# Kernel optimization log

Hardware: AMD Instinct MI355X
Metric: run time of the kernel (lower is better)

Reference implementation:

```python
import jax, jax.numpy as jnp
import numpy as np

D_MODEL, EMB_DIM, ORDER, SEQ_LEN, BATCH = 768, 33, 64, 8192, 2


def setup_inputs() -> dict:
    key = jax.random.key(0)
    ks = jax.random.split(key, 9)
    x = jax.random.normal(ks[0], (BATCH, D_MODEL, SEQ_LEN), dtype=jnp.float32)

    # PositionalEmbedding: t in [0,1], complex exponential bands
    bands = (EMB_DIM - 1) // 2
    t = jnp.linspace(0.0, 1.0, SEQ_LEN, dtype=jnp.float32)[None, :, None]          # (1, L, 1)
    t_rescaled = jnp.linspace(0.0, SEQ_LEN - 1, SEQ_LEN, dtype=jnp.float32)[None, :, None]
    w_ang = 2.0 * jnp.pi * t_rescaled / SEQ_LEN                                     # (1, L, 1)
    f = jnp.linspace(1e-4, bands - 1, bands, dtype=jnp.float32)[None, None]         # (1, 1, bands)
    zc = jnp.exp(-1j * f.astype(jnp.complex64) * w_ang.astype(jnp.complex64))
    z = jnp.concatenate([t, zc.real, zc.imag], axis=-1)                             # (1, L, emb_dim)

    # Sin activation frequency (shared single instance across all MLP layers), w=1
    freq = jnp.ones((1, ORDER), dtype=jnp.float32)

    def lin(k, fan_out, fan_in):
        s = 1.0 / np.sqrt(fan_in)
        return jax.random.normal(k, (fan_out, fan_in), dtype=jnp.float32) * s

    W1 = lin(ks[1], ORDER, EMB_DIM)
    b1 = jax.random.normal(ks[2], (ORDER,), dtype=jnp.float32) * 0.02
    W2 = lin(ks[3], ORDER, ORDER)
    b2 = jax.random.normal(ks[4], (ORDER,), dtype=jnp.float32) * 0.02
    W3 = lin(ks[5], ORDER, ORDER)
    b3 = jax.random.normal(ks[6], (ORDER,), dtype=jnp.float32) * 0.02
    Wout = lin(ks[7], D_MODEL, ORDER)  # no bias

    # ExponentialModulation deltas (deterministic buffer)
    target, fast_pct, slow_pct = 0.01, 0.3, 1.5
    max_decay = np.log(target) / fast_pct
    min_decay = np.log(target) / slow_pct
    deltas = jnp.linspace(min_decay, max_decay, D_MODEL, dtype=jnp.float32)[None, None]  # (1,1,d)

    bias_D = jax.random.normal(ks[8], (D_MODEL,), dtype=jnp.float32)

    return {"x": x, "L": SEQ_LEN, "z": z, "t": t, "freq": freq,
            "W1": W1, "b1": b1, "W2": W2, "b2": b2, "W3": W3, "b3": b3,
            "Wout": Wout, "deltas": deltas, "bias_D": bias_D}


def reference(x, L, z, t, freq, W1, b1, W2, b2, W3, b3, Wout, deltas, bias_D):
    zL, tL = z[:, :L], t[:, :L]                      # (1, L, emb_dim), (1, L, 1)
    # Implicit filter MLP with shared Sin activation
    h = jnp.sin(freq * (jnp.einsum('ble,oe->blo', zL, W1) + b1))
    h = jnp.sin(freq * (jnp.einsum('blo,po->blp', h, W2) + b2))
    h = jnp.sin(freq * (jnp.einsum('blo,po->blp', h, W3) + b3))
    h = jnp.einsum('blo,do->bld', h, Wout)           # (1, L, d_model)
    # Exponential modulation
    h = h * jnp.exp(-tL * jnp.abs(deltas))
    k = h[0].T                                       # (d_model, L)
    # FFT-based long convolution (fftconv_ref with gelu=False).
    # torch: k_f = rfft(k, n)/n ; y = irfft(u_f*k_f, n, norm='forward') == standard irfft(u_f*rfft(k,n), n)
    fft_size = 2 * L
    k_f = jnp.fft.rfft(k, n=fft_size)                # (d_model, n//2+1) complex
    u_f = jnp.fft.rfft(x, n=fft_size)                # (B, d_model, n//2+1)
    y = jnp.fft.irfft(u_f * k_f, n=fft_size)[..., :L]
    out = y + x * bias_D[:, None]
    return out.astype(x.dtype)
```

## Files before the change

### kernel.cpp

```cpp
#include <hip/hip_runtime.h>
#include <hip/hip_fp16.h>
#include <math.h>

#define D_MODEL 768
#define EMB 33
#define ORDER 64
#define SEQ 8192
#define BATCH 2
#define M 8192

#define PI_F 3.14159265358979323846f

#define IDX(a) ((a) + ((a) >> 4) + ((a) >> 7))
#define LDS_SZ 8768

__device__ __forceinline__ int rev13(int x) { return (int)(__brev((unsigned)x) >> 19); }

__device__ __constant__ float C8[8] = {
    1.f, 0.9238795325f, 0.7071067812f, 0.3826834324f,
    0.f, -0.3826834324f, -0.7071067812f, -0.9238795325f };
__device__ __constant__ float S8n[8] = {
    0.f, -0.3826834324f, -0.7071067812f, -0.9238795325f,
    -1.f, -0.9238795325f, -0.7071067812f, -0.3826834324f };
__device__ __constant__ float S8p[8] = {
    0.f, 0.3826834324f, 0.7071067812f, 0.9238795325f,
    1.f, 0.9238795325f, 0.7071067812f, 0.3826834324f };

__global__ __launch_bounds__(256) void mlp_kernel(
    const float* __restrict__ z, const float* __restrict__ freq,
    const float* __restrict__ W1, const float* __restrict__ b1,
    const float* __restrict__ W2, const float* __restrict__ b2,
    const float* __restrict__ W3, const float* __restrict__ b3,
    float* __restrict__ h3T)
{
    __shared__ float zt[33 * 72];
    __shared__ float h1[64 * 72];
    __shared__ float h2[64 * 72];
    __shared__ float Wb[64 * 68];
    __shared__ float sfr[64], sb[64];
    int t = threadIdx.x;
    int l0 = blockIdx.x * 64;

    for (int i = t; i < 64 * 33; i += 256) {
        int l = i / 33, e = i - l * 33;
        zt[e * 72 + l] = z[(size_t)(l0 + l) * 33 + e];
    }
    for (int i = t; i < 64 * 33; i += 256) {
        int o = i / 33, e = i - o * 33;
        Wb[e * 68 + o] = W1[i];
    }
    if (t < 64) { sfr[t] = freq[t]; sb[t] = b1[t]; }
    __syncthreads();

    int lx = t & 15, oy = t >> 4;
    float fr4[4], bi4[4], acc[4][4];
#pragma unroll
    for (int i = 0; i < 4; ++i) { fr4[i] = sfr[4 * oy + i]; bi4[i] = sb[4 * oy + i]; }
#pragma unroll
    for (int c = 0; c < 4; ++c)
#pragma unroll
        for (int i = 0; i < 4; ++i) acc[c][i] = bi4[i];
    for (int e = 0; e < 33; ++e) {
        float4 hv = *(const float4*)&zt[e * 72 + 4 * lx];
        float4 wv = *(const float4*)&Wb[e * 68 + 4 * oy];
        float h[4] = {hv.x, hv.y, hv.z, hv.w}, w[4] = {wv.x, wv.y, wv.z, wv.w};
#pragma unroll
        for (int c = 0; c < 4; ++c)
#pragma unroll
            for (int i = 0; i < 4; ++i) acc[c][i] = fmaf(h[c], w[i], acc[c][i]);
    }
#pragma unroll
    for (int i = 0; i < 4; ++i) {
        float4 v = make_float4(__sinf(fr4[i] * acc[0][i]), __sinf(fr4[i] * acc[1][i]),
                               __sinf(fr4[i] * acc[2][i]), __sinf(fr4[i] * acc[3][i]));
        *(float4*)&h1[(4 * oy + i) * 72 + 4 * lx] = v;
    }
    __syncthreads();

    for (int i = t; i < 4096; i += 256) {
        int o = i >> 6, q = i & 63;
        Wb[q * 68 + o] = W2[i];
    }
    if (t < 64) sb[t] = b2[t];
    __syncthreads();
#pragma unroll
    for (int i = 0; i < 4; ++i) bi4[i] = sb[4 * oy + i];
#pragma unroll
    for (int c = 0; c < 4; ++c)
#pragma unroll
        for (int i = 0; i < 4; ++i) acc[c][i] = bi4[i];
    for (int q = 0; q < 64; ++q) {
        float4 hv = *(const float4*)&h1[q * 72 + 4 * lx];
        float4 wv = *(const float4*)&Wb[q * 68 + 4 * oy];
        float h[4] = {hv.x, hv.y, hv.z, hv.w}, w[4] = {wv.x, wv.y, wv.z, wv.w};
#pragma unroll
        for (int c = 0; c < 4; ++c)
#pragma unroll
            for (int i = 0; i < 4; ++i) acc[c][i] = fmaf(h[c], w[i], acc[c][i]);
    }
#pragma unroll
    for (int i = 0; i < 4; ++i) {
        float4 v = make_float4(__sinf(fr4[i] * acc[0][i]), __sinf(fr4[i] * acc[1][i]),
                               __sinf(fr4[i] * acc[2][i]), __sinf(fr4[i] * acc[3][i]));
        *(float4*)&h2[(4 * oy + i) * 72 + 4 * lx] = v;
    }
    __syncthreads();

    for (int i = t; i < 4096; i += 256) {
        int o = i >> 6, q = i & 63;
        Wb[q * 68 + o] = W3[i];
    }
    if (t < 64) sb[t] = b3[t];
    __syncthreads();
#pragma unroll
    for (int i = 0; i < 4; ++i) bi4[i] = sb[4 * oy + i];
#pragma unroll
    for (int c = 0; c < 4; ++c)
#pragma unroll
        for (int i = 0; i < 4; ++i) acc[c][i] = bi4[i];
    for (int q = 0; q < 64; ++q) {
        float4 hv = *(const float4*)&h2[q * 72 + 4 * lx];
        float4 wv = *(const float4*)&Wb[q * 68 + 4 * oy];
        float h[4] = {hv.x, hv.y, hv.z, hv.w}, w[4] = {wv.x, wv.y, wv.z, wv.w};
#pragma unroll
        for (int c = 0; c < 4; ++c)
#pragma unroll
            for (int i = 0; i < 4; ++i) acc[c][i] = fmaf(h[c], w[i], acc[c][i]);
    }
#pragma unroll
    for (int i = 0; i < 4; ++i) {
        float4 v = make_float4(__sinf(fr4[i] * acc[0][i]), __sinf(fr4[i] * acc[1][i]),
                               __sinf(fr4[i] * acc[2][i]), __sinf(fr4[i] * acc[3][i]));
        *(float4*)&h3T[(size_t)(4 * oy + i) * SEQ + l0 + 4 * lx] = v;
    }
}

__global__ __launch_bounds__(256) void filt_kernel(
    const float* __restrict__ h3T, const float* __restrict__ Wout,
    const float* __restrict__ tvec, const float* __restrict__ deltas,
    float* __restrict__ kout)
{
    __shared__ float ht[64 * 132];
    __shared__ float wt[64 * 68];
    int t = threadIdx.x;
    int l0 = blockIdx.x * 128, d0 = blockIdx.y * 64;

    for (int i = t; i < 64 * 128; i += 256) {
        int o = i >> 7, l = i & 127;
        ht[o * 132 + l] = h3T[(size_t)o * SEQ + l0 + l];
    }
    for (int i = t; i < 4096; i += 256) {
        int dd = i >> 6, kk = i & 63;
        wt[kk * 68 + dd] = Wout[(size_t)(d0 + dd) * 64 + kk];
    }
    __syncthreads();

    int lx = t & 31, dy = t >> 5;
    float acc[4][8];
#pragma unroll
    for (int c = 0; c < 4; ++c)
#pragma unroll
        for (int i = 0; i < 8; ++i) acc[c][i] = 0.f;
    for (int kk = 0; kk < 64; ++kk) {
        float4 hv = *(const float4*)&ht[kk * 132 + 4 * lx];
        float4 w0 = *(const float4*)&wt[kk * 68 + 8 * dy];
        float4 w1 = *(const float4*)&wt[kk * 68 + 8 * dy + 4];
        float h[4] = {hv.x, hv.y, hv.z, hv.w};
        float w[8] = {w0.x, w0.y, w0.z, w0.w, w1.x, w1.y, w1.z, w1.w};
#pragma unroll
        for (int c = 0; c < 4; ++c)
#pragma unroll
            for (int i = 0; i < 8; ++i) acc[c][i] = fmaf(h[c], w[i], acc[c][i]);
    }

    float4 tl4 = *(const float4*)&tvec[l0 + 4 * lx];
    float tl[4] = {tl4.x, tl4.y, tl4.z, tl4.w};
    float del[8];
#pragma unroll
    for (int i = 0; i < 8; ++i) del[i] = fabsf(deltas[d0 + 8 * dy + i]);
#pragma unroll
    for (int i = 0; i < 8; ++i) {
        int d = d0 + 8 * dy + i;
        float4 v = make_float4(acc[0][i] * __expf(-tl[0] * del[i]),
                               acc[1][i] * __expf(-tl[1] * del[i]),
                               acc[2][i] * __expf(-tl[2] * del[i]),
                               acc[3][i] * __expf(-tl[3] * del[i]));
        *(float4*)&kout[(size_t)d * SEQ + l0 + 4 * lx] = v;
    }
}

template<int H>
__device__ __forceinline__ void fwd8(float2* A, int t)
{
    constexpr int H4 = H / 4;
    int j0 = t & (H4 - 1);
    float c1, s1;
    __sincosf((-PI_F / (float)H) * (float)j0, &s1, &c1);
#pragma unroll
    for (int gg = 0; gg < 2; ++gg) {
        int g = t + (gg << 9);
        int j = g & (H4 - 1);
        int i = ((g & ~(H4 - 1)) << 3) | j;
        float c1g = c1, s1g = s1;
        if (H4 > 512 && gg == 1) {
            const float cR = 0.9238795325f, sR = -0.3826834324f;
            c1g = c1 * cR - s1 * sR;
            s1g = s1 * cR + c1 * sR;
        }
        float c2 = c1g * c1g - s1g * s1g, s2 = 2.f * c1g * s1g;
        float c3 = c2 * c2 - s2 * s2,     s3 = 2.f * c2 * s2;
        float xr[8], xi[8];
        int ad[8];
#pragma unroll
        for (int m = 0; m < 8; ++m) {
            ad[m] = IDX(i + m * H4);
            float2 v = A[ad[m]];
            xr[m] = v.x; xi[m] = v.y;
        }
        const float r = 0.70710678118f;
        float twc[4], tws[4];
        twc[0] = c1g;             tws[0] = s1g;
        twc[1] = r * (c1g + s1g); tws[1] = r * (s1g - c1g);
        twc[2] = s1g;             tws[2] = -c1g;
        twc[3] = r * (s1g - c1g); tws[3] = -r * (c1g + s1g);
#pragma unroll
        for (int m = 0; m < 4; ++m) {
            float ur = xr[m] + xr[m + 4], ui = xi[m] + xi[m + 4];
            float dr = xr[m] - xr[m + 4], di = xi[m] - xi[m + 4];
            xr[m] = ur; xi[m] = ui;
            xr[m + 4] = dr * twc[m] - di * tws[m];
            xi[m + 4] = dr * tws[m] + di * twc[m];
        }
#pragma unroll
        for (int base = 0; base < 8; base += 4)
#pragma unroll
            for (int mm = 0; mm < 2; ++mm) {
                int a = base + mm, b = a + 2;
                float ur = xr[a] + xr[b], ui = xi[a] + xi[b];
                float dr = xr[a] - xr[b], di = xi[a] - xi[b];
                xr[a] = ur; xi[a] = ui;
                if (mm == 0) { xr[b] = dr * c2 - di * s2; xi[b] = dr * s2 + di * c2; }
                else         { xr[b] = dr * s2 + di * c2; xi[b] = di * s2 - dr * c2; }
            }
#pragma unroll
        for (int m = 0; m < 8; m += 2) {
            float ur = xr[m] + xr[m + 1], ui = xi[m] + xi[m + 1];
            float dr = xr[m] - xr[m + 1], di = xi[m] - xi[m + 1];
            xr[m] = ur; xi[m] = ui;
            xr[m + 1] = dr * c3 - di * s3; xi[m + 1] = dr * s3 + di * c3;
        }
#pragma unroll
        for (int m = 0; m < 8; ++m) A[ad[m]] = make_float2(xr[m], xi[m]);
    }
}

template<int H>
__device__ __forceinline__ void inv8(float2* A, int t)
{
    int j0 = t & (H - 1);
    float ct, st;
    __sincosf((PI_F / (float)(4 * H)) * (float)j0, &st, &ct);
#pragma unroll
    for (int gg = 0; gg < 2; ++gg) {
        int g = t + (gg << 9);
        int j = g & (H - 1);
        int i = ((g & ~(H - 1)) << 3) | j;
        float c = ct, s = st;
        if (H > 512 && gg == 1) {
            const float cR = 0.9238795325f, sR = 0.3826834324f;
            c = ct * cR - st * sR;
            s = st * cR + ct * sR;
        }
        float c2 = c * c - s * s, s2 = 2.f * c * s;
        float c4 = c2 * c2 - s2 * s2, s4 = 2.f * c2 * s2;
        float xr[8], xi[8]; int ad[8];
#pragma unroll
        for (int m = 0; m < 8; ++m) {
            ad[m] = IDX(i + m * H);
            float2 v = A[ad[m]];
            xr[m] = v.x; xi[m] = v.y;
        }
#pragma unroll
        for (int m = 0; m < 8; m += 2) {
            float tr = xr[m + 1] * c4 - xi[m + 1] * s4;
            float ti = xr[m + 1] * s4 + xi[m + 1] * c4;
            xr[m + 1] = xr[m] - tr; xi[m + 1] = xi[m] - ti;
            xr[m]     = xr[m] + tr; xi[m]     = xi[m] + ti;
        }
#pragma unroll
        for (int base = 0; base < 8; base += 4)
#pragma unroll
            for (int mm = 0; mm < 2; ++mm) {
                int a = base + mm, b = a + 2;
                float tr, ti;
                if (mm == 0) { tr = xr[b] * c2 - xi[b] * s2; ti = xr[b] * s2 + xi[b] * c2; }
                else         { tr = -(xr[b] * s2 + xi[b] * c2); ti = xr[b] * c2 - xi[b] * s2; }
                xr[b] = xr[a] - tr; xi[b] = xi[a] - ti;
                xr[a] = xr[a] + tr; xi[a] = xi[a] + ti;
            }
        const float r = 0.70710678118f;
        float t3c[4], t3s[4];
        t3c[0] = c;           t3s[0] = s;
        t3c[1] = r * (c - s); t3s[1] = r * (c + s);
        t3c[2] = -s;          t3s[2] = c;
        t3c[3] = -r * (c + s); t3s[3] = r * (c - s);
#pragma unroll
        for (int m = 0; m < 4; ++m) {
            float tr = xr[m + 4] * t3c[m] - xi[m + 4] * t3s[m];
            float ti = xr[m + 4] * t3s[m] + xi[m + 4] * t3c[m];
            xr[m + 4] = xr[m] - tr; xi[m + 4] = xi[m] - ti;
            xr[m]     = xr[m] + tr; xi[m]     = xi[m] + ti;
        }
#pragma unroll
        for (int m = 0; m < 8; ++m) A[ad[m]] = make_float2(xr[m], xi[m]);
    }
}

__device__ __forceinline__ void fft_fwd(float2* A, int t)
{
    fwd8<4096>(A, t); __syncthreads();
    fwd8<512>(A, t);  __syncthreads();
    fwd8<64>(A, t);   __syncthreads();
    {
        int pb = IDX(16 * t);
        float fr[16], fi[16];
#pragma unroll
        for (int e = 0; e < 16; ++e) { float2 v = A[pb + e]; fr[e] = v.x; fi[e] = v.y; }
#pragma unroll
        for (int k = 0; k < 8; ++k) {
            float cs = C8[k], sn = S8n[k];
            float arr = fr[k], aii = fi[k], brr = fr[k + 8], bii = fi[k + 8];
            fr[k] = arr + brr; fi[k] = aii + bii;
            float dr = arr - brr, di = aii - bii;
            fr[k + 8] = dr * cs - di * sn; fi[k + 8] = dr * sn + di * cs;
        }
#pragma unroll
        for (int b0 = 0; b0 < 16; b0 += 8)
#pragma unroll
            for (int k = 0; k < 4; ++k) {
                float cs = C8[2 * k], sn = S8n[2 * k];
                int i0 = b0 + k, i1 = i0 + 4;
                float arr = fr[i0], aii = fi[i0], brr = fr[i1], bii = fi[i1];
                fr[i0] = arr + brr; fi[i0] = aii + bii;
                float dr = arr - brr, di = aii - bii;
                fr[i1] = dr * cs - di * sn; fi[i1] = dr * sn + di * cs;
            }
#pragma unroll
        for (int b0 = 0; b0 < 16; b0 += 4)
#pragma unroll
            for (int k = 0; k < 2; ++k) {
                float cs = C8[4 * k], sn = S8n[4 * k];
                int i0 = b0 + k, i1 = i0 + 2;
                float arr = fr[i0], aii = fi[i0], brr = fr[i1], bii = fi[i1];
                fr[i0] = arr + brr; fi[i0] = aii + bii;
                float dr = arr - brr, di = aii - bii;
                fr[i1] = dr * cs - di * sn; fi[i1] = dr * sn + di * cs;
            }
#pragma unroll
        for (int b0 = 0; b0 < 16; b0 += 2) {
            float arr = fr[b0], aii = fi[b0], brr = fr[b0 + 1], bii = fi[b0 + 1];
            fr[b0] = arr + brr; fi[b0] = aii + bii;
            fr[b0 + 1] = arr - brr; fi[b0 + 1] = aii - bii;
        }
#pragma unroll
        for (int e = 0; e < 16; ++e) A[pb + e] = make_float2(fr[e], fi[e]);
        __syncthreads();
    }
}

__device__ __forceinline__ void fft_inv(float2* A, int t)
{
    {
        int pb = IDX(16 * t);
        float fr[16], fi[16];
#pragma unroll
        for (int e = 0; e < 16; ++e) { float2 v = A[pb + e]; fr[e] = v.x; fi[e] = v.y; }
#pragma unroll
        for (int b0 = 0; b0 < 16; b0 += 2) {
            float arr = fr[b0], aii = fi[b0], brr = fr[b0 + 1], bii = fi[b0 + 1];
            fr[b0] = arr + brr; fi[b0] = aii + bii;
            fr[b0 + 1] = arr - brr; fi[b0 + 1] = aii - bii;
        }
#pragma unroll
        for (int b0 = 0; b0 < 16; b0 += 4)
#pragma unroll
            for (int k = 0; k < 2; ++k) {
                float cs = C8[4 * k], sn = S8p[4 * k];
                int i0 = b0 + k, i1 = i0 + 2;
                float arr = fr[i0], aii = fi[i0], brr = fr[i1], bii = fi[i1];
                float tr = brr * cs - bii * sn, ti = brr * sn + bii * cs;
                fr[i0] = arr + tr; fi[i0] = aii + ti;
                fr[i1] = arr - tr; fi[i1] = aii - ti;
            }
#pragma unroll
        for (int b0 = 0; b0 < 16; b0 += 8)
#pragma unroll
            for (int k = 0; k < 4; ++k) {
                float cs = C8[2 * k], sn = S8p[2 * k];
                int i0 = b0 + k, i1 = i0 + 4;
                float arr = fr[i0], aii = fi[i0], brr = fr[i1], bii = fi[i1];
                float tr = brr * cs - bii * sn, ti = brr * sn + bii * cs;
                fr[i0] = arr + tr; fi[i0] = aii + ti;
                fr[i1] = arr - tr; fi[i1] = aii - ti;
            }
#pragma unroll
        for (int k = 0; k < 8; ++k) {
            float cs = C8[k], sn = S8p[k];
            float arr = fr[k], aii = fi[k], brr = fr[k + 8], bii = fi[k + 8];
            float tr = brr * cs - bii * sn, ti = brr * sn + bii * cs;
            fr[k] = arr + tr; fi[k] = aii + ti;
            fr[k + 8] = arr - tr; fi[k + 8] = aii - ti;
        }
#pragma unroll
        for (int e = 0; e < 16; ++e) A[pb + e] = make_float2(fr[e], fi[e]);
        __syncthreads();
    }
    inv8<16>(A, t);   __syncthreads();
    inv8<128>(A, t);  __syncthreads();
    inv8<1024>(A, t); __syncthreads();
}

__global__ __launch_bounds__(512, 4) void kf_kernel(
    float* outk, float* kb0, float* kb1)
{
    __shared__ float2 A[LDS_SZ];
    int t = threadIdx.x, d = blockIdx.x;
    const float* kp = outk + (size_t)d * SEQ;
    for (int n = t; n < 4096; n += 512) {
        A[IDX(n)] = ((const float2*)kp)[n];
    }
    for (int n = 4096 + t; n < M; n += 512) A[IDX(n)] = make_float2(0.f, 0.f);
    __syncthreads();
    fft_fwd(A, t);

    __half2* P0 = (__half2*)(kb0 + (size_t)d * SEQ);
    __half2* P1 = (__half2*)(kb1 + (size_t)d * SEQ);
    bool dup = (kb1 != kb0);
    float cs, sn;
    __sincosf(-PI_F * (float)t * (1.0f / 8192.0f), &sn, &cs);
    const float cRo = 0.9807852804f, sRo = -0.1950903220f;
    for (int j = t; j <= 4096; j += 512) {
        int jm = (M - j) & (M - 1);
        int p0 = rev13(j), p1 = rev13(jm);
        float2 z1 = A[IDX(p0)], z2 = A[IDX(p1)];
        float Ar_ = 0.5f * (z1.x + z2.x), Ai_ = 0.5f * (z1.y - z2.y);
        float Br_ = 0.5f * (z1.y + z2.y), Bi_ = 0.5f * (z2.x - z1.x);
        float wbr = cs * Br_ - sn * Bi_, wbi = cs * Bi_ + sn * Br_;
        float K1r = Ar_ + wbr, K1i = Ai_ + wbi;
        float K2r = Ar_ - wbr, K2i = -(Ai_ - wbi);
        if (j == 0) {
            __half2 v = __floats2half2_rn(K1r, K2r);
            P0[0] = v; if (dup) P1[0] = v;
        } else {
            __half2 v1 = __floats2half2_rn(K1r, K1i);
            P0[j] = v1; if (dup) P1[j] = v1;
            if (j != 4096) {
                __half2 v2 = __floats2half2_rn(K2r, K2i);
                P0[M - j] = v2; if (dup) P1[M - j] = v2;
            }
        }
        float cn = cs * cRo - sn * sRo; sn = sn * cRo + cs * sRo; cs = cn;
    }
}

__global__ __launch_bounds__(512, 4) void conv_kernel(
    const float* __restrict__ x, const float* __restrict__ bias,
    float* outk, const float* __restrict__ kbase, int kstride)
{
    __shared__ float2 A[LDS_SZ];
    int t = threadIdx.x, d = blockIdx.x, b = blockIdx.y;
    const float* xp = x + ((size_t)(b * D_MODEL + d)) * SEQ;
    float bd = bias[d];

#pragma unroll
    for (int idx = 0; idx < 8; ++idx) {
        int n = t + (idx << 9);
        A[IDX(n)] = ((const float2*)xp)[n];
    }
    for (int n = 4096 + t; n < M; n += 512) A[IDX(n)] = make_float2(0.f, 0.f);
    __syncthreads();
    fft_fwd(A, t);

    const __half2* P = (const __half2*)(kbase + (size_t)(b * kstride + d) * SEQ);
    float cs, sn;
    __sincosf(-PI_F * (float)t * (1.0f / 8192.0f), &sn, &cs);
    const float cRo = 0.9807852804f, sRo = -0.1950903220f;
    for (int j = t; j <= 4096; j += 512) {
        int jm = (M - j) & (M - 1);
        int p0 = rev13(j), p1 = rev13(jm);
        int q0 = IDX(p0), q1 = IDX(p1);
        float2 z1 = A[q0], z2 = A[q1];
        float Ar_ = 0.5f * (z1.x + z2.x), Ai_ = 0.5f * (z1.y - z2.y);
        float Br_ = 0.5f * (z1.y + z2.y), Bi_ = 0.5f * (z2.x - z1.x);
        float wbr = cs * Br_ - sn * Bi_, wbi = cs * Bi_ + sn * Br_;
        float U1r = Ar_ + wbr, U1i = Ai_ + wbi;
        float U2r = Ar_ - wbr, U2i = -(Ai_ - wbi);
        float K1r, K1i, K2r, K2i;
        if (j == 0) {
            __half2 v = P[0];
            K1r = __low2float(v) + bd;  K1i = 0.f;
            K2r = __high2float(v) + bd; K2i = 0.f;
        } else {
            __half2 v1 = P[j];
            __half2 v2 = P[M - j];
            K1r = __low2float(v1) + bd; K1i = __high2float(v1);
            K2r = __low2float(v2) + bd; K2i = __high2float(v2);
        }
        float P1r = U1r * K1r - U1i * K1i, P1i = U1r * K1i + U1i * K1r;
        float P2r = U2r * K2r - U2i * K2i, P2i = U2r * K2i + U2i * K2r;
        float Er = 0.5f * (P1r + P2r), Ei = 0.5f * (P1i - P2i);
        float Or = 0.5f * (P1r - P2r), Oi = 0.5f * (P1i + P2i);
        float G = cs * Oi - sn * Or;
        float H = cs * Or + sn * Oi;
        A[q0] = make_float2(Er - G, Ei + H);
        if (j != 0) A[q1] = make_float2(Er + G, -Ei + H);
        float cn = cs * cRo - sn * sRo; sn = sn * cRo + cs * sRo; cs = cn;
    }
    __syncthreads();
    fft_inv(A, t);

    const float invM = 1.0f / 8192.0f;
    float* op = outk + ((size_t)(b * D_MODEL + d)) * SEQ;
#pragma unroll
    for (int idx = 0; idx < 8; ++idx) {
        int n = t + (idx << 9);
        float2 v = A[IDX(n)];
        float2 ov;
        ov.x = v.x * invM;
        ov.y = v.y * invM;
        ((float2*)op)[n] = ov;
    }
}

extern "C" void kernel_launch(void* const* d_in, const int* in_sizes, int n_in,
                              void* d_out, int out_size, void* d_ws, size_t ws_size,
                              hipStream_t stream)
{
    (void)in_sizes; (void)n_in; (void)out_size;
    const float* x      = (const float*)d_in[0];
    const float* z      = (const float*)d_in[2];
    const float* tvec   = (const float*)d_in[3];
    const float* freq   = (const float*)d_in[4];
    const float* W1     = (const float*)d_in[5];
    const float* b1     = (const float*)d_in[6];
    const float* W2     = (const float*)d_in[7];
    const float* b2     = (const float*)d_in[8];
    const float* W3     = (const float*)d_in[9];
    const float* b3     = (const float*)d_in[10];
    const float* Wout   = (const float*)d_in[11];
    const float* deltas = (const float*)d_in[12];
    const float* bias   = (const float*)d_in[13];
    float* out = (float*)d_out;

    float* h3T = out + ((size_t)(2 * D_MODEL - 64) * SEQ);
    float* k   = out;

    const size_t kbytes = (size_t)D_MODEL * SEQ * sizeof(float);
    bool usews = (d_ws != nullptr) && (ws_size >= kbytes);
    float* kws = (float*)d_ws;
    float* kb0 = usews ? kws : out;
    float* kb1 = usews ? kws : out + (size_t)D_MODEL * SEQ;
    const float* kbase = usews ? kws : out;
    int kstride = usews ? 0 : D_MODEL;

    hipLaunchKernelGGL(mlp_kernel, dim3(SEQ / 64), dim3(256), 0, stream,
                       z, freq, W1, b1, W2, b2, W3, b3, h3T);
    hipLaunchKernelGGL(filt_kernel, dim3(SEQ / 128, D_MODEL / 64), dim3(256), 0, stream,
                       h3T, Wout, tvec, deltas, k);
    hipLaunchKernelGGL(kf_kernel, dim3(D_MODEL), dim3(512), 0, stream,
                       out, kb0, kb1);
    hipLaunchKernelGGL(conv_kernel, dim3(D_MODEL, BATCH), dim3(512), 0, stream,
                       x, bias, out, kbase, kstride);
}
```

Before: 232.3 us.

## Remap FFT stages so each wavefront owns contiguous 1024-point chunks, dropping block barriers

Reassigns threads in the later radix-8 and radix-16 FFT stages so that each 64-thread wavefront works only on its own contiguous 1024-element chunk of LDS. The three stages after the first forward pass (and the first three inverse stages) then run without block-wide __syncthreads between them, which cuts four barriers per FFT pair. It relies on wavefront-level lockstep execution for LDS ordering within a wave, which is only safe if the wave size is 64 and the compiler does not reorder the LDS accesses.

```diff
diff --git a/kernel.cpp b/kernel.cpp
--- a/kernel.cpp
+++ b/kernel.cpp
@@ -190,138 +190,126 @@
 }
 
 template<int H>
-__device__ __forceinline__ void fwd8(float2* A, int t)
+__device__ __forceinline__ void fwd8g1(float2* A, int i, float c1, float s1)
 {
     constexpr int H4 = H / 4;
-    int j0 = t & (H4 - 1);
-    float c1, s1;
-    __sincosf((-PI_F / (float)H) * (float)j0, &s1, &c1);
-#pragma unroll
-    for (int gg = 0; gg < 2; ++gg) {
-        int g = t + (gg << 9);
-        int j = g & (H4 - 1);
-        int i = ((g & ~(H4 - 1)) << 3) | j;
-        float c1g = c1, s1g = s1;
-        if (H4 > 512 && gg == 1) {
-            const float cR = 0.9238795325f, sR = -0.3826834324f;
-            c1g = c1 * cR - s1 * sR;
-            s1g = s1 * cR + c1 * sR;
-        }
-        float c2 = c1g * c1g - s1g * s1g, s2 = 2.f * c1g * s1g;
-        float c3 = c2 * c2 - s2 * s2,     s3 = 2.f * c2 * s2;
-        float xr[8], xi[8];
-        int ad[8];
-#pragma unroll
-        for (int m = 0; m < 8; ++m) {
-            ad[m] = IDX(i + m * H4);
-            float2 v = A[ad[m]];
-            xr[m] = v.x; xi[m] = v.y;
-        }
-        const float r = 0.70710678118f;
-        float twc[4], tws[4];
-        twc[0] = c1g;             tws[0] = s1g;
-        twc[1] = r * (c1g + s1g); tws[1] = r * (s1g - c1g);
-        twc[2] = s1g;             tws[2] = -c1g;
-        twc[3] = r * (s1g - c1g); tws[3] = -r * (c1g + s1g);
-#pragma unroll
-        for (int m = 0; m < 4; ++m) {
-            float ur = xr[m] + xr[m + 4], ui = xi[m] + xi[m + 4];
-            float dr = xr[m] - xr[m + 4], di = xi[m] - xi[m + 4];
-            xr[m] = ur; xi[m] = ui;
-            xr[m + 4] = dr * twc[m] - di * tws[m];
-            xi[m + 4] = dr * tws[m] + di * twc[m];
-        }
-#pragma unroll
-        for (int base = 0; base < 8; base += 4)
-#pragma unroll
-            for (int mm = 0; mm < 2; ++mm) {
-                int a = base + mm, b = a + 2;
-                float ur = xr[a] + xr[b], ui = xi[a] + xi[b];
-                float dr = xr[a] - xr[b], di = xi[a] - xi[b];
-                xr[a] = ur; xi[a] = ui;
-                if (mm == 0) { xr[b] = dr * c2 - di * s2; xi[b] = dr * s2 + di * c2; }
-                else         { xr[b] = dr * s2 + di * c2; xi[b] = di * s2 - dr * c2; }
-            }
-#pragma unroll
-        for (int m = 0; m < 8; m += 2) {
-            float ur = xr[m] + xr[m + 1], ui = xi[m] + xi[m + 1];
-            float dr = xr[m] - xr[m + 1], di = xi[m] - xi[m + 1];
-            xr[m] = ur; xi[m] = ui;
-            xr[m + 1] = dr * c3 - di * s3; xi[m + 1] = dr * s3 + di * c3;
-        }
-#pragma unroll
-        for (int m = 0; m < 8; ++m) A[ad[m]] = make_float2(xr[m], xi[m]);
-    }
+    float c2 = c1 * c1 - s1 * s1, s2 = 2.f * c1 * s1;
+    float c3 = c2 * c2 - s2 * s2, s3 = 2.f * c2 * s2;
+    float xr[8], xi[8];
+    int ad[8];
+#pragma unroll
+    for (int m = 0; m < 8; ++m) {
+        ad[m] = IDX(i + m * H4);
+        float2 v = A[ad[m]];
+        xr[m] = v.x; xi[m] = v.y;
+    }
+    const float r = 0.70710678118f;
+    float twc[4], tws[4];
+    twc[0] = c1;            tws[0] = s1;
+    twc[1] = r * (c1 + s1); tws[1] = r * (s1 - c1);
+    twc[2] = s1;            tws[2] = -c1;
+    twc[3] = r * (s1 - c1); tws[3] = -r * (c1 + s1);
+#pragma unroll
+    for (int m = 0; m < 4; ++m) {
+        float ur = xr[m] + xr[m + 4], ui = xi[m] + xi[m + 4];
+        float dr = xr[m] - xr[m + 4], di = xi[m] - xi[m + 4];
+        xr[m] = ur; xi[m] = ui;
+        xr[m + 4] = dr * twc[m] - di * tws[m];
+        xi[m + 4] = dr * tws[m] + di * twc[m];
+    }
+#pragma unroll
+    for (int base = 0; base < 8; base += 4)
+#pragma unroll
+        for (int mm = 0; mm < 2; ++mm) {
+            int a = base + mm, b = a + 2;
+            float ur = xr[a] + xr[b], ui = xi[a] + xi[b];
+            float dr = xr[a] - xr[b], di = xi[a] - xi[b];
+            xr[a] = ur; xi[a] = ui;
+            if (mm == 0) { xr[b] = dr * c2 - di * s2; xi[b] = dr * s2 + di * c2; }
+            else         { xr[b] = dr * s2 + di * c2; xi[b] = di * s2 - dr * c2; }
+        }
+#pragma unroll
+    for (int m = 0; m < 8; m += 2) {
+        float ur = xr[m] + xr[m + 1], ui = xi[m] + xi[m + 1];
+        float dr = xr[m] - xr[m + 1], di = xi[m] - xi[m + 1];
+        xr[m] = ur; xi[m] = ui;
+        xr[m + 1] = dr * c3 - di * s3; xi[m + 1] = dr * s3 + di * c3;
+    }
+#pragma unroll
+    for (int m = 0; m < 8; ++m) A[ad[m]] = make_float2(xr[m], xi[m]);
 }
 
 template<int H>
-__device__ __forceinline__ void inv8(float2* A, int t)
-{
-    int j0 = t & (H - 1);
-    float ct, st;
-    __sincosf((PI_F / (float)(4 * H)) * (float)j0, &st, &ct);
-#pragma unroll
-    for (int gg = 0; gg < 2; ++gg) {
-        int g = t + (gg << 9);
-        int j = g & (H - 1);
-        int i = ((g & ~(H - 1)) << 3) | j;
-        float c = ct, s = st;
-        if (H > 512 && gg == 1) {
-            const float cR = 0.9238795325f, sR = 0.3826834324f;
-            c = ct * cR - st * sR;
-            s = st * cR + ct * sR;
-        }
-        float c2 = c * c - s * s, s2 = 2.f * c * s;
-        float c4 = c2 * c2 - s2 * s2, s4 = 2.f * c2 * s2;
-        float xr[8], xi[8]; int ad[8];
-#pragma unroll
-        for (int m = 0; m < 8; ++m) {
-            ad[m] = IDX(i + m * H);
-            float2 v = A[ad[m]];
-            xr[m] = v.x; xi[m] = v.y;
-        }
-#pragma unroll
-        for (int m = 0; m < 8; m += 2) {
-            float tr = xr[m + 1] * c4 - xi[m + 1] * s4;
-            float ti = xr[m + 1] * s4 + xi[m + 1] * c4;
-            xr[m + 1] = xr[m] - tr; xi[m + 1] = xi[m] - ti;
-            xr[m]     = xr[m] + tr; xi[m]     = xi[m] + ti;
-        }
-#pragma unroll
-        for (int base = 0; base < 8; base += 4)
-#pragma unroll
-            for (int mm = 0; mm < 2; ++mm) {
-                int a = base + mm, b = a + 2;
-                float tr, ti;
-                if (mm == 0) { tr = xr[b] * c2 - xi[b] * s2; ti = xr[b] * s2 + xi[b] * c2; }
-                else         { tr = -(xr[b] * s2 + xi[b] * c2); ti = xr[b] * c2 - xi[b] * s2; }
-                xr[b] = xr[a] - tr; xi[b] = xi[a] - ti;
-                xr[a] = xr[a] + tr; xi[a] = xi[a] + ti;
-            }
-        const float r = 0.70710678118f;
-        float t3c[4], t3s[4];
-        t3c[0] = c;           t3s[0] = s;
-        t3c[1] = r * (c - s); t3s[1] = r * (c + s);
-        t3c[2] = -s;          t3s[2] = c;
-        t3c[3] = -r * (c + s); t3s[3] = r * (c - s);
-#pragma unroll
-        for (int m = 0; m < 4; ++m) {
-            float tr = xr[m + 4] * t3c[m] - xi[m + 4] * t3s[m];
-            float ti = xr[m + 4] * t3s[m] + xi[m + 4] * t3c[m];
-            xr[m + 4] = xr[m] - tr; xi[m + 4] = xi[m] - ti;
-            xr[m]     = xr[m] + tr; xi[m]     = xi[m] + ti;
-        }
-#pragma unroll
-        for (int m = 0; m < 8; ++m) A[ad[m]] = make_float2(xr[m], xi[m]);
-    }
+__device__ __forceinline__ void inv8g1(float2* A, int i, float c, float s)
+{
+    float c2 = c * c - s * s, s2 = 2.f * c * s;
+    float c4 = c2 * c2 - s2 * s2, s4 = 2.f * c2 * s2;
+    float xr[8], xi[8]; int ad[8];
+#pragma unroll
+    for (int m = 0; m < 8; ++m) {
+        ad[m] = IDX(i + m * H);
+        float2 v = A[ad[m]];
+        xr[m] = v.x; xi[m] = v.y;
+    }
+#pragma unroll
+    for (int m = 0; m < 8; m += 2) {
+        float tr = xr[m + 1] * c4 - xi[m + 1] * s4;
+        float ti = xr[m + 1] * s4 + xi[m + 1] * c4;
+        xr[m + 1] = xr[m] - tr; xi[m + 1] = xi[m] - ti;
+        xr[m]     = xr[m] + tr; xi[m]     = xi[m] + ti;
+    }
+#pragma unroll
+    for (int base = 0; base < 8; base += 4)
+#pragma unroll
+        for (int mm = 0; mm < 2; ++mm) {
+            int a = base + mm, b = a + 2;
+            float tr, ti;
+            if (mm == 0) { tr = xr[b] * c2 - xi[b] * s2; ti = xr[b] * s2 + xi[b] * c2; }
+            else         { tr = -(xr[b] * s2 + xi[b] * c2); ti = xr[b] * c2 - xi[b] * s2; }
+            xr[b] = xr[a] - tr; xi[b] = xi[a] - ti;
+            xr[a] = xr[a] + tr; xi[a] = xi[a] + ti;
+        }
+    const float r = 0.70710678118f;
+    float t3c[4], t3s[4];
+    t3c[0] = c;            t3s[0] = s;
+    t3c[1] = r * (c - s);  t3s[1] = r * (c + s);
+    t3c[2] = -s;           t3s[2] = c;
+    t3c[3] = -r * (c + s); t3s[3] = r * (c - s);
+#pragma unroll
+    for (int m = 0; m < 4; ++m) {
+        float tr = xr[m + 4] * t3c[m] - xi[m + 4] * t3s[m];
+        float ti = xr[m + 4] * t3s[m] + xi[m + 4] * t3c[m];
+        xr[m + 4] = xr[m] - tr; xi[m + 4] = xi[m] - ti;
+        xr[m]     = xr[m] + tr; xi[m]     = xi[m] + ti;
+    }
+#pragma unroll
+    for (int m = 0; m < 8; ++m) A[ad[m]] = make_float2(xr[m], xi[m]);
 }
 
 __device__ __forceinline__ void fft_fwd(float2* A, int t)
 {
-    fwd8<4096>(A, t); __syncthreads();
-    fwd8<512>(A, t);  __syncthreads();
-    fwd8<64>(A, t);   __syncthreads();
     {
+        float c1, s1;
+        __sincosf((-PI_F / 4096.0f) * (float)t, &s1, &c1);
+        fwd8g1<4096>(A, t, c1, s1);
+        const float cR = 0.9238795325f, sR = -0.3826834324f;
+        fwd8g1<4096>(A, t + 512, c1 * cR - s1 * sR, s1 * cR + c1 * sR);
+    }
+    __syncthreads();
+    {
+        int w = t >> 6, l = t & 63, base = w << 10;
+        float ca, sa;
+        __sincosf((-PI_F / 512.0f) * (float)l, &sa, &ca);
+        fwd8g1<512>(A, base + l, ca, sa);
+        const float cR = 0.9238795325f, sR = -0.3826834324f;
+        fwd8g1<512>(A, base + 64 + l, ca * cR - sa * sR, sa * cR + ca * sR);
+
+        float cb, sb;
+        __sincosf((-PI_F / 64.0f) * (float)(l & 15), &sb, &cb);
+        int i0 = base + ((l & ~15) << 3) + (l & 15);
+        fwd8g1<64>(A, i0, cb, sb);
+        fwd8g1<64>(A, i0 + 512, cb, sb);
+
         int pb = IDX(16 * t);
         float fr[16], fi[16];
 #pragma unroll
@@ -339,22 +327,22 @@
 #pragma unroll
             for (int k = 0; k < 4; ++k) {
                 float cs = C8[2 * k], sn = S8n[2 * k];
-                int i0 = b0 + k, i1 = i0 + 4;
-                float arr = fr[i0], aii = fi[i0], brr = fr[i1], bii = fi[i1];
-                fr[i0] = arr + brr; fi[i0] = aii + bii;
+                int i1 = b0 + k, i2 = i1 + 4;
+                float arr = fr[i1], aii = fi[i1], brr = fr[i2], bii = fi[i2];
+                fr[i1] = arr + brr; fi[i1] = aii + bii;
                 float dr = arr - brr, di = aii - bii;
-                fr[i1] = dr * cs - di * sn; fi[i1] = dr * sn + di * cs;
+                fr[i2] = dr * cs - di * sn; fi[i2] = dr * sn + di * cs;
             }
 #pragma unroll
         for (int b0 = 0; b0 < 16; b0 += 4)
 #pragma unroll
             for (int k = 0; k < 2; ++k) {
                 float cs = C8[4 * k], sn = S8n[4 * k];
-                int i0 = b0 + k, i1 = i0 + 2;
-                float arr = fr[i0], aii = fi[i0], brr = fr[i1], bii = fi[i1];
-                fr[i0] = arr + brr; fi[i0] = aii + bii;
+                int i1 = b0 + k, i2 = i1 + 2;
+                float arr = fr[i1], aii = fi[i1], brr = fr[i2], bii = fi[i2];
+                fr[i1] = arr + brr; fi[i1] = aii + bii;
                 float dr = arr - brr, di = aii - bii;
-                fr[i1] = dr * cs - di * sn; fi[i1] = dr * sn + di * cs;
+                fr[i2] = dr * cs - di * sn; fi[i2] = dr * sn + di * cs;
             }
 #pragma unroll
         for (int b0 = 0; b0 < 16; b0 += 2) {
@@ -364,8 +352,8 @@
         }
 #pragma unroll
         for (int e = 0; e < 16; ++e) A[pb + e] = make_float2(fr[e], fi[e]);
-        __syncthreads();
-    }
+    }
+    __syncthreads();
 }
 
 __device__ __forceinline__ void fft_inv(float2* A, int t)
@@ -386,22 +374,22 @@
 #pragma unroll
             for (int k = 0; k < 2; ++k) {
                 float cs = C8[4 * k], sn = S8p[4 * k];
-                int i0 = b0 + k, i1 = i0 + 2;
-                float arr = fr[i0], aii = fi[i0], brr = fr[i1], bii = fi[i1];
+                int i1 = b0 + k, i2 = i1 + 2;
+                float arr = fr[i1], aii = fi[i1], brr = fr[i2], bii = fi[i2];
                 float tr = brr * cs - bii * sn, ti = brr * sn + bii * cs;
-                fr[i0] = arr + tr; fi[i0] = aii + ti;
-                fr[i1] = arr - tr; fi[i1] = aii - ti;
+                fr[i1] = arr + tr; fi[i1] = aii + ti;
+                fr[i2] = arr - tr; fi[i2] = aii - ti;
             }
 #pragma unroll
         for (int b0 = 0; b0 < 16; b0 += 8)
 #pragma unroll
             for (int k = 0; k < 4; ++k) {
                 float cs = C8[2 * k], sn = S8p[2 * k];
-                int i0 = b0 + k, i1 = i0 + 4;
-                float arr = fr[i0], aii = fi[i0], brr = fr[i1], bii = fi[i1];
+                int i1 = b0 + k, i2 = i1 + 4;
+                float arr = fr[i1], aii = fi[i1], brr = fr[i2], bii = fi[i2];
                 float tr = brr * cs - bii * sn, ti = brr * sn + bii * cs;
-                fr[i0] = arr + tr; fi[i0] = aii + ti;
-                fr[i1] = arr - tr; fi[i1] = aii - ti;
+                fr[i1] = arr + tr; fi[i1] = aii + ti;
+                fr[i2] = arr - tr; fi[i2] = aii - ti;
             }
 #pragma unroll
         for (int k = 0; k < 8; ++k) {
@@ -413,11 +401,29 @@
         }
 #pragma unroll
         for (int e = 0; e < 16; ++e) A[pb + e] = make_float2(fr[e], fi[e]);
-        __syncthreads();
-    }
-    inv8<16>(A, t);   __syncthreads();
-    inv8<128>(A, t);  __syncthreads();
-    inv8<1024>(A, t); __syncthreads();
+
+        int w = t >> 6, l = t & 63, base = w << 10;
+        float ca, sa;
+        __sincosf((PI_F / 64.0f) * (float)(l & 15), &sa, &ca);
+        int i0 = base + ((l & ~15) << 3) + (l & 15);
+        inv8g1<16>(A, i0, ca, sa);
+        inv8g1<16>(A, i0 + 512, ca, sa);
+
+        float cb, sb;
+        __sincosf((PI_F / 512.0f) * (float)l, &sb, &cb);
+        inv8g1<128>(A, base + l, cb, sb);
+        const float cR = 0.9238795325f, sR = 0.3826834324f;
+        inv8g1<128>(A, base + 64 + l, cb * cR - sb * sR, sb * cR + cb * sR);
+    }
+    __syncthreads();
+    {
+        float c1, s1;
+        __sincosf((PI_F / 4096.0f) * (float)t, &s1, &c1);
+        inv8g1<1024>(A, t, c1, s1);
+        const float cR = 0.9238795325f, sR = 0.3826834324f;
+        inv8g1<1024>(A, t + 512, c1 * cR - s1 * sR, s1 * cR + c1 * sR);
+    }
+    __syncthreads();
 }
 
 __global__ __launch_bounds__(512, 4) void kf_kernel(
```

Measured after the change: 230.5 us. Within noise of the previous version (-0.8%).
